# Performance work log

Measured on AMD Instinct MI355X. Metric: run time of the kernel, lower is better.

Reference implementation:

```python
import jax, jax.numpy as jnp
import numpy as np

N2 = 524288   # raw batch (2B)
F = 256       # raw feature dim; concat of halves -> D = 2F
D = 512       # input_dim (gated feature dim)
H_GATE = 64
H_EXP = 128


def _init(key, shape, fan_in):
    return jax.random.normal(key, shape, jnp.float32) / np.sqrt(fan_in)


def setup_inputs() -> dict:
    key = jax.random.key(0)
    ks = jax.random.split(key, 13)
    x = jax.random.normal(ks[0], (N2, F), jnp.float32)
    # gate: Linear(D,64) -> ReLU -> Linear(64,2)
    gw1 = _init(ks[1], (D, H_GATE), D)
    gb1 = jnp.zeros((H_GATE,), jnp.float32)
    gw2 = _init(ks[2], (H_GATE, 2), H_GATE)
    gb2 = jnp.zeros((2,), jnp.float32)
    # expert_a: Linear(D,128) -> ReLU -> Linear(128,2)
    aw1 = _init(ks[3], (D, H_EXP), D)
    ab1 = jnp.zeros((H_EXP,), jnp.float32)
    aw2 = _init(ks[4], (H_EXP, 2), H_EXP)
    ab2 = jnp.zeros((2,), jnp.float32)
    # expert_b: same shapes
    bw1 = _init(ks[5], (D, H_EXP), D)
    bb1 = jnp.zeros((H_EXP,), jnp.float32)
    bw2 = _init(ks[6], (H_EXP, 2), H_EXP)
    bb2 = jnp.zeros((2,), jnp.float32)
    return dict(x=x, gw1=gw1, gb1=gb1, gw2=gw2, gb2=gb2,
                aw1=aw1, ab1=ab1, aw2=aw2, ab2=ab2,
                bw1=bw1, bb1=bb1, bw2=bw2, bb2=bb2)


def reference(x, gw1, gb1, gw2, gb2, aw1, ab1, aw2, ab2, bw1, bb1, bw2, bb2):
    # backbone = identity; concat first and second batch halves along features
    n = x.shape[0]
    xf = jnp.concatenate([x[: n // 2], x[n // 2 :]], axis=1)  # [B, D]
    # hard gate: argmax over 2 logits
    gate_logits = jax.nn.relu(xf @ gw1 + gb1) @ gw2 + gb2  # [B, 2]
    gate_idx = jnp.argmax(gate_logits, axis=1)  # [B]
    # run both tiny experts densely, then mask (same math as masked dispatch)
    out_a = jax.nn.relu(xf @ aw1 + ab1) @ aw2 + ab2  # [B, 2]
    out_b = jax.nn.relu(xf @ bw1 + bb1) @ bw2 + bb2  # [B, 2]
    m_a = (gate_idx == 0)[:, None]
    # rows routed to expert_a fill cols 0:2, rows routed to expert_b fill cols 2:4
    return jnp.concatenate(
        [jnp.where(m_a, out_a, 0.0), jnp.where(m_a, 0.0, out_b)], axis=1
    )  # [B, 4]
```

## Files before the change

### kernel.cpp

```cpp
#include <hip/hip_runtime.h>
#include <hip/hip_bf16.h>

#define HALF_ROWS 262144
#define TAU 0.04f
#define BT_OFF 1024
#define LIST_OFF (BT_OFF + 320 * 512 * 2)

typedef __attribute__((ext_vector_type(8))) short s16x8;
typedef __attribute__((ext_vector_type(8))) unsigned short u16x8;
typedef __attribute__((ext_vector_type(4))) float f32x4;

__device__ __forceinline__ unsigned short f2bf(float f) {
  union { float f; unsigned u; } v; v.f = f;
  unsigned r = v.u + 0x7fffu + ((v.u >> 16) & 1u);
  return (unsigned short)(r >> 16);
}

#define GLOAD_LDS16(g, p) \
  __builtin_amdgcn_global_load_lds((const __attribute__((address_space(1))) void*)(g), \
                                   (__attribute__((address_space(3))) void*)(p), 16, 0, 0)

__global__ void moe_prep(const float* __restrict__ gw1, const float* __restrict__ aw1,
                         const float* __restrict__ bw1, unsigned short* __restrict__ Bf,
                         unsigned* __restrict__ cnt) {
  if (blockIdx.x == 0 && threadIdx.x == 0) *cnt = 0u;
  int idx = blockIdx.x * 512 + threadIdx.x;
  int j = idx & 7, l = (idx >> 3) & 63, ks = (idx >> 9) & 15, cb = idx >> 13;
  int col = cb * 16 + (l & 15);
  int k = ks * 32 + ((l >> 4) << 3) + j;
  float v;
  if (col < 64)       v = gw1[k * 64 + col];
  else if (col < 192) v = aw1[k * 128 + (col - 64)];
  else                v = bw1[k * 128 + (col - 192)];
  Bf[idx] = f2bf(v);
}

__global__ __launch_bounds__(512, 4) void moe_main(
    const float* __restrict__ x, const unsigned short* __restrict__ Bf,
    const float* __restrict__ gb1, const float* __restrict__ gw2, const float* __restrict__ gb2,
    const float* __restrict__ ab1, const float* __restrict__ aw2, const float* __restrict__ ab2,
    const float* __restrict__ bb1, const float* __restrict__ bw2, const float* __restrict__ bb2,
    float* __restrict__ out, unsigned* __restrict__ cnt, unsigned* __restrict__ list, int cap) {
  __shared__ char L[49152];
  char* ALb = L;
  char* BLb = L + 8192;
  float* part = (float*)L;

  const int tid = threadIdx.x;
  const int bid = blockIdx.x;
  const int w = tid >> 6, l = tid & 63;
  const int wr = w >> 2, wc = w & 3;
  const int lo = l & 15, hi = l >> 4;
  const long br = (long)bid * 64;

  const int arow = ((tid >> 7) << 4) + (tid & 15);
  const int akl  = ((tid >> 6) & 1) * 32 + ((tid >> 4) & 3) * 8;

  f32x4 sa0, sa1;
  auto issueA = [&](int kc) {
    const float* p = x + ((long)(kc >= 4 ? HALF_ROWS : 0) + br + arow) * 256
                       + (kc & 3) * 64 + akl;
    sa0 = *(const f32x4*)p;
    sa1 = *(const f32x4*)(p + 4);
  };
  auto commitA = [&]() {
    u16x8 u;
    const float* s0 = (const float*)&sa0;
    const float* s1 = (const float*)&sa1;
#pragma unroll
    for (int i = 0; i < 4; ++i) { u[i] = f2bf(s0[i]); u[4 + i] = f2bf(s1[i]); }
    *(u16x8*)(ALb + (size_t)tid * 16) = u;
  };

  f32x4 acc[2][5];
#pragma unroll
  for (int i = 0; i < 2; i++)
#pragma unroll
    for (int j = 0; j < 5; j++) acc[i][j] = (f32x4){0.f, 0.f, 0.f, 0.f};

  issueA(0);

#pragma unroll 1
  for (int kc = 0; kc < 8; ++kc) {
#pragma unroll
    for (int s5 = 0; s5 < 5; ++s5) {
      int s = w * 5 + s5;
      const unsigned short* g = Bf + ((size_t)(((s >> 1) * 16 + kc * 2 + (s & 1)) * 64 + l)) * 8;
      GLOAD_LDS16(g, BLb + (size_t)s * 1024);
    }
    asm volatile("" ::: "memory");
    commitA();
    if (kc < 7) {
      issueA(kc + 1);
      asm volatile("s_waitcnt vmcnt(2) lgkmcnt(0)" ::: "memory");
    } else {
      asm volatile("s_waitcnt vmcnt(0) lgkmcnt(0)" ::: "memory");
    }
    __builtin_amdgcn_s_barrier();

#pragma unroll
    for (int ks = 0; ks < 2; ++ks) {
      s16x8 afr[2], bfr[5];
#pragma unroll
      for (int rt = 0; rt < 2; ++rt)
        afr[rt] = *(const s16x8*)(ALb + (size_t)((((wr * 2 + rt) * 2 + ks) * 64 + l)) * 16);
#pragma unroll
      for (int ct = 0; ct < 5; ++ct)
        bfr[ct] = *(const s16x8*)(BLb + (size_t)((((wc * 5 + ct) * 2 + ks) * 64 + l)) * 16);
#pragma unroll
      for (int rt = 0; rt < 2; ++rt)
#pragma unroll
        for (int ct = 0; ct < 5; ++ct)
          acc[rt][ct] = __builtin_amdgcn_mfma_f32_16x16x32_bf16(
              afr[rt], bfr[ct], acc[rt][ct], 0, 0, 0);
    }
    asm volatile("" ::: "memory");
    __builtin_amdgcn_s_barrier();
  }

  float b1v[5], w0v[5], w1v[5];
  int head[5];
#pragma unroll
  for (int ct = 0; ct < 5; ++ct) {
    int c0 = (wc * 5 + ct) * 16;
    int col = c0 + lo;
    int hd = c0 < 64 ? 0 : (c0 < 192 ? 1 : 2);
    head[ct] = hd;
    if (hd == 0)      { b1v[ct] = gb1[col];           w0v[ct] = gw2[col * 2];       w1v[ct] = gw2[col * 2 + 1]; }
    else if (hd == 1) { int c = col - 64;  b1v[ct] = ab1[c]; w0v[ct] = aw2[c * 2]; w1v[ct] = aw2[c * 2 + 1]; }
    else              { int c = col - 192; b1v[ct] = bb1[c]; w0v[ct] = bw2[c * 2]; w1v[ct] = bw2[c * 2 + 1]; }
  }
#pragma unroll
  for (int rt = 0; rt < 2; ++rt) {
    float pg0[4] = {0,0,0,0}, pg1[4] = {0,0,0,0};
    float pa0[4] = {0,0,0,0}, pa1[4] = {0,0,0,0};
    float pq0[4] = {0,0,0,0}, pq1[4] = {0,0,0,0};
#pragma unroll
    for (int ct = 0; ct < 5; ++ct)
#pragma unroll
      for (int j = 0; j < 4; ++j) {
        float h = fmaxf(acc[rt][ct][j] + b1v[ct], 0.f);
        float t0 = h * w0v[ct], t1 = h * w1v[ct];
        if (head[ct] == 0)      { pg0[j] += t0; pg1[j] += t1; }
        else if (head[ct] == 1) { pa0[j] += t0; pa1[j] += t1; }
        else                    { pq0[j] += t0; pq1[j] += t1; }
      }
#pragma unroll
    for (int m = 1; m < 16; m <<= 1)
#pragma unroll
      for (int j = 0; j < 4; ++j) {
        pg0[j] += __shfl_xor(pg0[j], m); pg1[j] += __shfl_xor(pg1[j], m);
        pa0[j] += __shfl_xor(pa0[j], m); pa1[j] += __shfl_xor(pa1[j], m);
        pq0[j] += __shfl_xor(pq0[j], m); pq1[j] += __shfl_xor(pq1[j], m);
      }
    if (lo == 0) {
#pragma unroll
      for (int j = 0; j < 4; ++j) {
        int r = wr * 32 + rt * 16 + hi * 4 + j;
        float* pp = part + (r * 4 + wc) * 6;
        pp[0] = pg0[j]; pp[1] = pg1[j]; pp[2] = pa0[j];
        pp[3] = pa1[j]; pp[4] = pq0[j]; pp[5] = pq1[j];
      }
    }
  }
  __syncthreads();

  if (tid < 64) {
    float g0 = 0, g1 = 0, a0 = 0, a1 = 0, e0 = 0, e1 = 0;
#pragma unroll
    for (int k2 = 0; k2 < 4; k2++) {
      float* pp = part + (tid * 4 + k2) * 6;
      g0 += pp[0]; g1 += pp[1]; a0 += pp[2]; a1 += pp[3]; e0 += pp[4]; e1 += pp[5];
    }
    float gl0 = g0 + gb2[0], gl1 = g1 + gb2[1];
    float fa0 = a0 + ab2[0], fa1 = a1 + ab2[1];
    float fb0 = e0 + bb2[0], fb1 = e1 + bb2[1];
    bool m0 = gl0 >= gl1;
    long grow = br + tid;
    f32x4 o;
    o[0] = m0 ? fa0 : 0.f; o[1] = m0 ? fa1 : 0.f;
    o[2] = m0 ? 0.f : fb0; o[3] = m0 ? 0.f : fb1;
    *(f32x4*)(out + grow * 4) = o;
    float diff = gl0 - gl1;
    if (fabsf(diff) < TAU && cap > 0) {
      unsigned u = atomicAdd(cnt, 1u);
      if (u < (unsigned)cap) {
        unsigned* e = list + (size_t)u * 8;
        e[0] = (unsigned)grow;
        float* ef = (float*)(e + 4);
        ef[0] = fa0; ef[1] = fa1; ef[2] = fb0; ef[3] = fb1;
      }
    }
  }
}

__global__ void moe_fixup(const float* __restrict__ x,
                          const float* __restrict__ gw1, const float* __restrict__ gb1,
                          const float* __restrict__ gw2, const float* __restrict__ gb2,
                          float* __restrict__ out, const unsigned* __restrict__ cnt,
                          const unsigned* __restrict__ list, int cap) {
  unsigned n = *cnt;
  if (n > (unsigned)cap) n = (unsigned)cap;
  const int l = threadIdx.x & 63;
  const int wid = blockIdx.x * (blockDim.x >> 6) + (threadIdx.x >> 6);
  const int nw = gridDim.x * (blockDim.x >> 6);
  for (unsigned e = wid; e < n; e += nw) {
    const unsigned* ent = list + (size_t)e * 8;
    unsigned row = ent[0];
    const float* ef = (const float*)(ent + 4);
    const float* xr0 = x + (long)row * 256;
    const float* xr1 = x + ((long)row + HALF_ROWS) * 256;
    double a0 = 0.0, a1 = 0.0, a2 = 0.0, a3 = 0.0;
#pragma unroll 4
    for (int d = 0; d < 256; d += 4) {
      a0 += (double)xr0[d]     * (double)gw1[d * 64 + l];
      a1 += (double)xr0[d + 1] * (double)gw1[(d + 1) * 64 + l];
      a2 += (double)xr0[d + 2] * (double)gw1[(d + 2) * 64 + l];
      a3 += (double)xr0[d + 3] * (double)gw1[(d + 3) * 64 + l];
    }
#pragma unroll 4
    for (int d = 0; d < 256; d += 4) {
      a0 += (double)xr1[d]     * (double)gw1[(d + 256) * 64 + l];
      a1 += (double)xr1[d + 1] * (double)gw1[(d + 257) * 64 + l];
      a2 += (double)xr1[d + 2] * (double)gw1[(d + 258) * 64 + l];
      a3 += (double)xr1[d + 3] * (double)gw1[(d + 259) * 64 + l];
    }
    double h = a0 + a1 + a2 + a3 + (double)gb1[l];
    h = h > 0.0 ? h : 0.0;
    double t0 = h * (double)gw2[l * 2];
    double t1 = h * (double)gw2[l * 2 + 1];
#pragma unroll
    for (int m = 1; m < 64; m <<= 1) {
      t0 += __shfl_xor(t0, m);
      t1 += __shfl_xor(t1, m);
    }
    if (l == 0) {
      bool m0 = (t0 + (double)gb2[0]) >= (t1 + (double)gb2[1]);
      f32x4 o;
      o[0] = m0 ? ef[0] : 0.f; o[1] = m0 ? ef[1] : 0.f;
      o[2] = m0 ? 0.f : ef[2]; o[3] = m0 ? 0.f : ef[3];
      *(f32x4*)(out + (size_t)row * 4) = o;
    }
  }
}

extern "C" void kernel_launch(void* const* d_in, const int* in_sizes, int n_in,
                              void* d_out, int out_size, void* d_ws, size_t ws_size,
                              hipStream_t stream) {
  const float* x   = (const float*)d_in[0];
  const float* gw1 = (const float*)d_in[1];
  const float* gb1 = (const float*)d_in[2];
  const float* gw2 = (const float*)d_in[3];
  const float* gb2 = (const float*)d_in[4];
  const float* aw1 = (const float*)d_in[5];
  const float* ab1 = (const float*)d_in[6];
  const float* aw2 = (const float*)d_in[7];
  const float* ab2 = (const float*)d_in[8];
  const float* bw1 = (const float*)d_in[9];
  const float* bb1 = (const float*)d_in[10];
  const float* bw2 = (const float*)d_in[11];
  const float* bb2 = (const float*)d_in[12];
  float* out = (float*)d_out;

  unsigned char* ws = (unsigned char*)d_ws;
  unsigned* cnt = (unsigned*)ws;
  unsigned short* Bf = (unsigned short*)(ws + BT_OFF);
  unsigned* list = (unsigned*)(ws + LIST_OFF);
  long cap_l = ((long)ws_size - (long)LIST_OFF) / 32;
  int cap = cap_l < 0 ? 0 : (cap_l > 262144 ? 262144 : (int)cap_l);

  moe_prep<<<320, 512, 0, stream>>>(gw1, aw1, bw1, Bf, cnt);
  moe_main<<<4096, 512, 0, stream>>>(x, Bf, gb1, gw2, gb2, ab1, aw2, ab2,
                                     bb1, bw2, bb2, out, cnt, list, cap);
  moe_fixup<<<1024, 256, 0, stream>>>(x, gw1, gb1, gw2, gb2, out, cnt, list, cap);
}
```

Baseline: 307.2 us.

## Load A fragments directly to registers and multi-buffer B in LDS

The activation tile no longer goes through LDS. Each lane loads its MFMA A-fragment straight from global memory and converts it with packed hardware bf16 conversion instructions. The weight tile now streams through a 4-deep LDS ring with two chunks prefetched ahead, so each iteration needs one waitcnt+barrier instead of two barriers. LDS use rises to 80KB per block, which may lower occupancy, and the hand-tuned vmcnt thresholds are fragile.

```diff
diff --git a/kernel.cpp b/kernel.cpp
--- a/kernel.cpp
+++ b/kernel.cpp
@@ -7,7 +7,6 @@
 #define LIST_OFF (BT_OFF + 320 * 512 * 2)
 
 typedef __attribute__((ext_vector_type(8))) short s16x8;
-typedef __attribute__((ext_vector_type(8))) unsigned short u16x8;
 typedef __attribute__((ext_vector_type(4))) float f32x4;
 
 __device__ __forceinline__ unsigned short f2bf(float f) {
@@ -19,6 +18,17 @@
 #define GLOAD_LDS16(g, p) \
   __builtin_amdgcn_global_load_lds((const __attribute__((address_space(1))) void*)(g), \
                                    (__attribute__((address_space(3))) void*)(p), 16, 0, 0)
+
+#define WB(N) asm volatile("s_waitcnt vmcnt(" #N ")\n\ts_barrier" ::: "memory")
+
+__device__ __forceinline__ s16x8 cvt8(const f32x4& a, const f32x4& b) {
+  union { int i[4]; s16x8 v; } u;
+  asm("v_cvt_pk_bf16_f32 %0, %1, %2" : "=v"(u.i[0]) : "v"(a[0]), "v"(a[1]));
+  asm("v_cvt_pk_bf16_f32 %0, %1, %2" : "=v"(u.i[1]) : "v"(a[2]), "v"(a[3]));
+  asm("v_cvt_pk_bf16_f32 %0, %1, %2" : "=v"(u.i[2]) : "v"(b[0]), "v"(b[1]));
+  asm("v_cvt_pk_bf16_f32 %0, %1, %2" : "=v"(u.i[3]) : "v"(b[2]), "v"(b[3]));
+  return u.v;
+}
 
 __global__ void moe_prep(const float* __restrict__ gw1, const float* __restrict__ aw1,
                          const float* __restrict__ bw1, unsigned short* __restrict__ Bf,
@@ -41,81 +51,66 @@
     const float* __restrict__ ab1, const float* __restrict__ aw2, const float* __restrict__ ab2,
     const float* __restrict__ bb1, const float* __restrict__ bw2, const float* __restrict__ bb2,
     float* __restrict__ out, unsigned* __restrict__ cnt, unsigned* __restrict__ list, int cap) {
-  __shared__ char L[49152];
-  char* ALb = L;
-  char* BLb = L + 8192;
+  __shared__ char L[81920];
   float* part = (float*)L;
 
   const int tid = threadIdx.x;
-  const int bid = blockIdx.x;
   const int w = tid >> 6, l = tid & 63;
   const int wr = w >> 2, wc = w & 3;
   const int lo = l & 15, hi = l >> 4;
-  const long br = (long)bid * 64;
-
-  const int arow = ((tid >> 7) << 4) + (tid & 15);
-  const int akl  = ((tid >> 6) & 1) * 32 + ((tid >> 4) & 3) * 8;
-
-  f32x4 sa0, sa1;
+  const long br = (long)blockIdx.x * 64;
+
+  const float* xb0 = x + (br + wr * 32 + lo) * 256 + hi * 8;
+  const float* xb1 = xb0 + 16 * 256;
+
+  const int sb = (w * 20) >> 3, se = ((w + 1) * 20) >> 3;
+  const unsigned short* bsrc = Bf + l * 8;
+
+  f32x4 n0a, n0b, n1a, n1b;
   auto issueA = [&](int kc) {
-    const float* p = x + ((long)(kc >= 4 ? HALF_ROWS : 0) + br + arow) * 256
-                       + (kc & 3) * 64 + akl;
-    sa0 = *(const f32x4*)p;
-    sa1 = *(const f32x4*)(p + 4);
+    const long off = (long)(kc & 7) * 32 + (kc >= 8 ? (long)HALF_ROWS * 256 : 0L);
+    const float* p0 = xb0 + off;
+    const float* p1 = xb1 + off;
+    n0a = *(const f32x4*)p0; n0b = *(const f32x4*)(p0 + 4);
+    n1a = *(const f32x4*)p1; n1b = *(const f32x4*)(p1 + 4);
   };
-  auto commitA = [&]() {
-    u16x8 u;
-    const float* s0 = (const float*)&sa0;
-    const float* s1 = (const float*)&sa1;
-#pragma unroll
-    for (int i = 0; i < 4; ++i) { u[i] = f2bf(s0[i]); u[4 + i] = f2bf(s1[i]); }
-    *(u16x8*)(ALb + (size_t)tid * 16) = u;
+  auto issueB = [&](int kc) {
+    char* dst = L + (kc & 3) * 20480;
+    const unsigned short* g = bsrc + kc * 512;
+    for (int s = sb; s < se; ++s)
+      GLOAD_LDS16(g + s * 8192, dst + s * 1024);
   };
 
-  f32x4 acc[2][5];
-#pragma unroll
-  for (int i = 0; i < 2; i++)
-#pragma unroll
-    for (int j = 0; j < 5; j++) acc[i][j] = (f32x4){0.f, 0.f, 0.f, 0.f};
+  f32x4 acc0[5], acc1[5];
+#pragma unroll
+  for (int j = 0; j < 5; j++) {
+    acc0[j] = (f32x4){0.f, 0.f, 0.f, 0.f};
+    acc1[j] = (f32x4){0.f, 0.f, 0.f, 0.f};
+  }
 
   issueA(0);
+  issueB(0);
+  issueB(1);
 
 #pragma unroll 1
-  for (int kc = 0; kc < 8; ++kc) {
-#pragma unroll
-    for (int s5 = 0; s5 < 5; ++s5) {
-      int s = w * 5 + s5;
-      const unsigned short* g = Bf + ((size_t)(((s >> 1) * 16 + kc * 2 + (s & 1)) * 64 + l)) * 8;
-      GLOAD_LDS16(g, BLb + (size_t)s * 1024);
-    }
+  for (int kc = 0; kc < 16; ++kc) {
+    s16x8 a0 = cvt8(n0a, n0b);
+    s16x8 a1 = cvt8(n1a, n1b);
     asm volatile("" ::: "memory");
-    commitA();
-    if (kc < 7) {
-      issueA(kc + 1);
-      asm volatile("s_waitcnt vmcnt(2) lgkmcnt(0)" ::: "memory");
-    } else {
-      asm volatile("s_waitcnt vmcnt(0) lgkmcnt(0)" ::: "memory");
-    }
-    __builtin_amdgcn_s_barrier();
-
-#pragma unroll
-    for (int ks = 0; ks < 2; ++ks) {
-      s16x8 afr[2], bfr[5];
-#pragma unroll
-      for (int rt = 0; rt < 2; ++rt)
-        afr[rt] = *(const s16x8*)(ALb + (size_t)((((wr * 2 + rt) * 2 + ks) * 64 + l)) * 16);
-#pragma unroll
-      for (int ct = 0; ct < 5; ++ct)
-        bfr[ct] = *(const s16x8*)(BLb + (size_t)((((wc * 5 + ct) * 2 + ks) * 64 + l)) * 16);
-#pragma unroll
-      for (int rt = 0; rt < 2; ++rt)
-#pragma unroll
-        for (int ct = 0; ct < 5; ++ct)
-          acc[rt][ct] = __builtin_amdgcn_mfma_f32_16x16x32_bf16(
-              afr[rt], bfr[ct], acc[rt][ct], 0, 0, 0);
-    }
+    if (kc < 15) issueA(kc + 1);
+    if (kc < 14) issueB(kc + 2);
     asm volatile("" ::: "memory");
-    __builtin_amdgcn_s_barrier();
+    if (kc < 14)       { if (w & 1) WB(10); else WB(8); }
+    else if (kc == 14) { if (w & 1) WB(7);  else WB(6); }
+    else               { WB(0); }
+
+    const char* buf = L + (kc & 3) * 20480;
+#pragma unroll
+    for (int ct = 0; ct < 5; ++ct) {
+      s16x8 bf = *(const s16x8*)(buf + ((wc * 5 + ct) << 10) + (l << 4));
+      acc0[ct] = __builtin_amdgcn_mfma_f32_16x16x32_bf16(a0, bf, acc0[ct], 0, 0, 0);
+      acc1[ct] = __builtin_amdgcn_mfma_f32_16x16x32_bf16(a1, bf, acc1[ct], 0, 0, 0);
+    }
   }
 
   float b1v[5], w0v[5], w1v[5];
@@ -130,39 +125,43 @@
     else if (hd == 1) { int c = col - 64;  b1v[ct] = ab1[c]; w0v[ct] = aw2[c * 2]; w1v[ct] = aw2[c * 2 + 1]; }
     else              { int c = col - 192; b1v[ct] = bb1[c]; w0v[ct] = bw2[c * 2]; w1v[ct] = bw2[c * 2 + 1]; }
   }
-#pragma unroll
-  for (int rt = 0; rt < 2; ++rt) {
-    float pg0[4] = {0,0,0,0}, pg1[4] = {0,0,0,0};
-    float pa0[4] = {0,0,0,0}, pa1[4] = {0,0,0,0};
-    float pq0[4] = {0,0,0,0}, pq1[4] = {0,0,0,0};
-#pragma unroll
-    for (int ct = 0; ct < 5; ++ct)
-#pragma unroll
-      for (int j = 0; j < 4; ++j) {
-        float h = fmaxf(acc[rt][ct][j] + b1v[ct], 0.f);
-        float t0 = h * w0v[ct], t1 = h * w1v[ct];
-        if (head[ct] == 0)      { pg0[j] += t0; pg1[j] += t1; }
-        else if (head[ct] == 1) { pa0[j] += t0; pa1[j] += t1; }
-        else                    { pq0[j] += t0; pq1[j] += t1; }
-      }
-#pragma unroll
-    for (int m = 1; m < 16; m <<= 1)
-#pragma unroll
-      for (int j = 0; j < 4; ++j) {
-        pg0[j] += __shfl_xor(pg0[j], m); pg1[j] += __shfl_xor(pg1[j], m);
-        pa0[j] += __shfl_xor(pa0[j], m); pa1[j] += __shfl_xor(pa1[j], m);
-        pq0[j] += __shfl_xor(pq0[j], m); pq1[j] += __shfl_xor(pq1[j], m);
-      }
-    if (lo == 0) {
-#pragma unroll
-      for (int j = 0; j < 4; ++j) {
-        int r = wr * 32 + rt * 16 + hi * 4 + j;
-        float* pp = part + (r * 4 + wc) * 6;
-        pp[0] = pg0[j]; pp[1] = pg1[j]; pp[2] = pa0[j];
-        pp[3] = pa1[j]; pp[4] = pq0[j]; pp[5] = pq1[j];
-      }
-    }
-  }
+
+#define EPI(ACC, RT)                                                              \
+  {                                                                               \
+    float pg0[4] = {0,0,0,0}, pg1[4] = {0,0,0,0};                                 \
+    float pa0[4] = {0,0,0,0}, pa1[4] = {0,0,0,0};                                 \
+    float pq0[4] = {0,0,0,0}, pq1[4] = {0,0,0,0};                                 \
+    _Pragma("unroll")                                                             \
+    for (int ct = 0; ct < 5; ++ct)                                                \
+      _Pragma("unroll")                                                           \
+      for (int j = 0; j < 4; ++j) {                                               \
+        float h = fmaxf(ACC[ct][j] + b1v[ct], 0.f);                               \
+        float t0 = h * w0v[ct], t1 = h * w1v[ct];                                 \
+        if (head[ct] == 0)      { pg0[j] += t0; pg1[j] += t1; }                   \
+        else if (head[ct] == 1) { pa0[j] += t0; pa1[j] += t1; }                   \
+        else                    { pq0[j] += t0; pq1[j] += t1; }                   \
+      }                                                                           \
+    _Pragma("unroll")                                                             \
+    for (int m = 1; m < 16; m <<= 1)                                              \
+      _Pragma("unroll")                                                           \
+      for (int j = 0; j < 4; ++j) {                                               \
+        pg0[j] += __shfl_xor(pg0[j], m); pg1[j] += __shfl_xor(pg1[j], m);         \
+        pa0[j] += __shfl_xor(pa0[j], m); pa1[j] += __shfl_xor(pa1[j], m);         \
+        pq0[j] += __shfl_xor(pq0[j], m); pq1[j] += __shfl_xor(pq1[j], m);         \
+      }                                                                           \
+    if (lo == 0) {                                                                \
+      _Pragma("unroll")                                                           \
+      for (int j = 0; j < 4; ++j) {                                               \
+        int r = wr * 32 + (RT) * 16 + hi * 4 + j;                                 \
+        float* pp = part + (r * 4 + wc) * 6;                                      \
+        pp[0] = pg0[j]; pp[1] = pg1[j]; pp[2] = pa0[j];                           \
+        pp[3] = pa1[j]; pp[4] = pq0[j]; pp[5] = pq1[j];                           \
+      }                                                                           \
+    }                                                                             \
+  }
+
+  EPI(acc0, 0)
+  EPI(acc1, 1)
   __syncthreads();
 
   if (tid < 64) {
```

After: 400.2 us. 30.3% more time.
